# Kernel tuning notes

Hardware: AMD Instinct MI355X
Metric: run time of the kernel (lower is better)

Reference implementation:

```python
import jax, jax.numpy as jnp
import numpy as np

B, T, IN, H = 16, 256, 512, 1024
G = 4 * H  # gates: i, f, g, o (PyTorch order)
N_LAYERS = 8  # lstm1 (4 layers) + lstm2 (4 layers), all hidden=1024


def lstm_layer(x, Wih, Whh, bih, bhh):
    # x: [B,T,D_in]; Wih: [4H,D_in]; Whh: [4H,H]; biases: [4H]
    xg = jnp.einsum('btd,gd->btg', x, Wih) + bih + bhh  # precompute input proj [B,T,4H]
    b = x.shape[0]

    def step(carry, xg_t):
        h, c = carry
        g = xg_t + h @ Whh.T  # [B,4H]
        i, f, gg, o = jnp.split(g, 4, axis=-1)
        c = jax.nn.sigmoid(f) * c + jax.nn.sigmoid(i) * jnp.tanh(gg)
        h = jax.nn.sigmoid(o) * jnp.tanh(c)
        return (h, c), h

    init = (jnp.zeros((b, H), x.dtype), jnp.zeros((b, H), x.dtype))
    _, hs = jax.lax.scan(step, init, jnp.swapaxes(xg, 0, 1))  # [T,B,H]
    return jnp.swapaxes(hs, 0, 1)


def setup_inputs() -> dict:
    key = jax.random.key(0)
    ks = jax.random.split(key, 16)
    s = 1.0 / np.sqrt(H)  # PyTorch LSTM uniform init scale
    u = lambda k, shp: jax.random.uniform(k, shp, jnp.float32, -s, s)
    return {
        'x': jax.random.normal(ks[0], (B, T, IN), jnp.float32),
        'W_ih0': u(ks[1], (G, IN)),            # layer 0 input proj
        'W_ih_rest': u(ks[2], (N_LAYERS - 1, G, H)),  # layers 1..7
        'W_hh': u(ks[3], (N_LAYERS, G, H)),
        'b_ih': u(ks[4], (N_LAYERS, G)),
        'b_hh': u(ks[5], (N_LAYERS, G)),
        'fc1_w': u(ks[6], (512, H)), 'fc1_b': u(ks[7], (512,)),
        'fc2_w': u(ks[8], (256, 512)), 'fc2_b': u(ks[9], (256,)),
        'fc3_w': u(ks[10], (1, 256)), 'fc3_b': u(ks[11], (1,)),
    }


def reference(x, W_ih0, W_ih_rest, W_hh, b_ih, b_hh,
              fc1_w, fc1_b, fc2_w, fc2_b, fc3_w, fc3_b):
    # 8 stacked LSTM layers (dropout = identity in eval mode)
    h = lstm_layer(x, W_ih0, W_hh[0], b_ih[0], b_hh[0])
    for l in range(1, N_LAYERS):
        h = lstm_layer(h, W_ih_rest[l - 1], W_hh[l], b_ih[l], b_hh[l])
    out = h[:, -1, :]  # last timestep [B,H]
    out = jax.nn.relu(out @ fc1_w.T + fc1_b)
    out = jax.nn.relu(out @ fc2_w.T + fc2_b)
    return out @ fc3_w.T + fc3_b  # [B,1]
```

## Files before the change

### kernel.cpp

```cpp
#include <hip/hip_runtime.h>

constexpr int BB = 16;
constexpr int TT = 256;
constexpr int IN0 = 512;
constexpr int HH = 1024;
constexpr int GG = 4096;
constexpr int NLAYERS = 8;

constexpr size_t XG_OFF   = 0;
constexpr size_t REG0_OFF = 67108864;
constexpr size_t REG1_OFF = REG0_OFF + 16777216;
constexpr size_t HE_OFF   = REG1_OFF + 16777216;
constexpr size_t HO_OFF   = HE_OFF + 262144;
constexpr size_t FC1_OFF  = HO_OFF + 262144;
constexpr size_t FC2_OFF  = FC1_OFF + 32768;
constexpr size_t BAR_OFF  = FC2_OFF + 16384;

constexpr int BLO_B  = 69632;
constexpr int PART_F = 34816;
constexpr int SMEM_BYTES = 147968;

typedef __attribute__((ext_vector_type(8))) short bf16x8;
typedef __attribute__((ext_vector_type(4))) float f32x4;

__device__ __forceinline__ unsigned short f2bf(float f)
{
    union { float f; unsigned u; } v{f};
    unsigned r = v.u + 0x7FFFu + ((v.u >> 16) & 1u);
    return (unsigned short)(r >> 16);
}
__device__ __forceinline__ float bf2f(unsigned short h)
{
    union { unsigned u; float f; } v{(unsigned)h << 16};
    return v.f;
}

__global__ __launch_bounds__(256) void conv_split(const float* __restrict__ in,
                                                  ushort* __restrict__ oh,
                                                  ushort* __restrict__ ol, int n4)
{
    int g = blockIdx.x * blockDim.x + threadIdx.x;
    if (g >= n4) return;
    float4 f = ((const float4*)in)[g];
    ushort4 h, l;
    h.x = f2bf(f.x); l.x = f2bf(f.x - bf2f(h.x));
    h.y = f2bf(f.y); l.y = f2bf(f.y - bf2f(h.y));
    h.z = f2bf(f.z); l.z = f2bf(f.z - bf2f(h.z));
    h.w = f2bf(f.w); l.w = f2bf(f.w - bf2f(h.w));
    ((ushort4*)oh)[g] = h;
    ((ushort4*)ol)[g] = l;
}

__global__ __launch_bounds__(256) void gemm_mfma(const ushort* __restrict__ Ah,
                                                 const ushort* __restrict__ Al,
                                                 const ushort* __restrict__ Wh,
                                                 const ushort* __restrict__ Wl,
                                                 const float* __restrict__ bih,
                                                 const float* __restrict__ bhh,
                                                 float* __restrict__ out, int K)
{
    __shared__ ushort lds[2][128 * 72];
    const int tid = threadIdx.x;
    const int w = tid >> 6, ln = tid & 63;
    const int m0 = blockIdx.y * 128, n0 = blockIdx.x * 128;
    const int arow = (w >> 1) * 64, bcol = (w & 1) * 64;
    const int lm = ln & 15, lk = (ln >> 4) * 8;
    const int sr = tid >> 3, sc = (tid & 7) * 8;

    f32x4 acc[4][4] = {};

#pragma unroll
    for (int s = 0; s < 3; ++s) {
        const ushort* Asrc = (s < 2) ? Ah : Al;
        const ushort* Bsrc = (s == 1) ? Wl : Wh;
        for (int k0 = 0; k0 < K; k0 += 64) {
            __syncthreads();
#pragma unroll
            for (int i = 0; i < 4; ++i) {
                int r = sr + 32 * i;
                *(uint4*)&lds[0][r * 72 + sc] =
                    *(const uint4*)(Asrc + (size_t)(m0 + r) * K + k0 + sc);
                *(uint4*)&lds[1][r * 72 + sc] =
                    *(const uint4*)(Bsrc + (size_t)(n0 + r) * K + k0 + sc);
            }
            __syncthreads();
#pragma unroll
            for (int ks = 0; ks < 2; ++ks) {
                bf16x8 af[4], bf[4];
#pragma unroll
                for (int i = 0; i < 4; ++i)
                    af[i] = *(const bf16x8*)&lds[0][(arow + i * 16 + lm) * 72 + ks * 32 + lk];
#pragma unroll
                for (int j = 0; j < 4; ++j)
                    bf[j] = *(const bf16x8*)&lds[1][(bcol + j * 16 + lm) * 72 + ks * 32 + lk];
#pragma unroll
                for (int i = 0; i < 4; ++i)
#pragma unroll
                    for (int j = 0; j < 4; ++j)
                        acc[i][j] = __builtin_amdgcn_mfma_f32_16x16x32_bf16(
                            af[i], bf[j], acc[i][j], 0, 0, 0);
            }
        }
    }

#pragma unroll
    for (int j = 0; j < 4; ++j) {
        const int n = n0 + bcol + j * 16 + lm;
        const float bsum = bih[n] + bhh[n];
#pragma unroll
        for (int i = 0; i < 4; ++i) {
            const int mrow = m0 + arow + i * 16 + (ln >> 4) * 4;
#pragma unroll
            for (int r = 0; r < 4; ++r) {
                const int m = mrow + r;
                const int bb = m >> 8, tt = m & 255;
                out[(size_t)(tt * 16 + bb) * GG + n] = acc[i][j][r] + bsum;
            }
        }
    }
}

__device__ __forceinline__ float sigf(float x) { return 1.0f / (1.0f + expf(-x)); }

__global__ __launch_bounds__(512, 1) void scan_pair(
    const float* __restrict__ WhhE, const float* __restrict__ WhhO,
    const float* __restrict__ WihO, const float* __restrict__ xg,
    ushort* __restrict__ hseq_hi, ushort* __restrict__ hseq_lo,
    unsigned* __restrict__ hEbuf, unsigned* __restrict__ hObuf,
    const float* __restrict__ bihO, const float* __restrict__ bhhO,
    unsigned* __restrict__ barE, unsigned* __restrict__ barO,
    unsigned base)
{
    extern __shared__ float smem[];
    char* smb = (char*)smem;
    const int tid  = threadIdx.x;
    const int wgid = blockIdx.x;
    const int half = wgid >> 7, lwg = wgid & 127;
    const int j0 = lwg << 3;
    const int w = tid >> 6, ln = tid & 63;
    const int m = ln & 15, kq = ln >> 4;
    const int t_w = w & 1, s_w = w >> 1;
    const int grp = lwg >> 4;

    unsigned* myBar = half ? barO : barE;
    unsigned* otBar = half ? barE : barO;
    unsigned* myH   = half ? hObuf : hEbuf;

    bf16x8 wf_hi[8], wf_lo[8];
    {
        const int r = t_w * 16 + m;
        const int grow = ((r >> 3) << 10) + j0 + (r & 7);
        const float* wrow = (half ? WhhO : WhhE) + (size_t)grow * 1024 + (s_w << 8) + (kq << 3);
#pragma unroll
        for (int s = 0; s < 8; ++s) {
            float4 f0 = *(const float4*)(wrow + s * 32);
            float4 f1 = *(const float4*)(wrow + s * 32 + 4);
            float fv[8] = {f0.x, f0.y, f0.z, f0.w, f1.x, f1.y, f1.z, f1.w};
            bf16x8 h8, l8;
#pragma unroll
            for (int i = 0; i < 8; ++i) {
                unsigned short hb = f2bf(fv[i]);
                h8[i] = (short)hb;
                l8[i] = (short)f2bf(fv[i] - bf2f(hb));
            }
            wf_hi[s] = h8; wf_lo[s] = l8;
        }
    }
    bf16x8 uf_hi[8], uf_lo[8];
    if (half) {
        const int r = t_w * 16 + m;
        const int grow = ((r >> 3) << 10) + j0 + (r & 7);
        const float* wrow = WihO + (size_t)grow * 1024 + (s_w << 8) + (kq << 3);
#pragma unroll
        for (int s = 0; s < 8; ++s) {
            float4 f0 = *(const float4*)(wrow + s * 32);
            float4 f1 = *(const float4*)(wrow + s * 32 + 4);
            float fv[8] = {f0.x, f0.y, f0.z, f0.w, f1.x, f1.y, f1.z, f1.w};
            bf16x8 h8, l8;
#pragma unroll
            for (int i = 0; i < 8; ++i) {
                unsigned short hb = f2bf(fv[i]);
                h8[i] = (short)hb;
                l8[i] = (short)f2bf(fv[i] - bf2f(hb));
            }
            uf_hi[s] = h8; uf_lo[s] = l8;
        }
    }

    const int bidx = ln >> 4, jj = ln & 15;
    const int kkloc = jj >> 1, sub = (jj & 1) * 8;
    const int q = tid >> 4, bg = tid & 15;

    float cs0 = 0.f, cs1 = 0.f;
    float2 gin[4] = {};
    if (tid < 64) {
        if (half) {
#pragma unroll
            for (int g = 0; g < 4; ++g) {
                const int c0 = g * 1024 + j0 + 2 * q;
                gin[g] = make_float2(bihO[c0] + bhhO[c0], bihO[c0 + 1] + bhhO[c0 + 1]);
            }
        } else {
#pragma unroll
            for (int g = 0; g < 4; ++g)
                gin[g] = *(const float2*)(xg + (size_t)bg * GG + g * 1024 + j0 + 2 * q);
        }
    }

    for (int t = 0; t < TT; ++t) {
        const unsigned gt = base + (unsigned)t;
        if (tid == 0) {
            if (t > 0) {
                unsigned* p = myBar + 512 + (grp << 4);
                while (__hip_atomic_load(p, __ATOMIC_RELAXED, __HIP_MEMORY_SCOPE_AGENT) < gt)
                    __builtin_amdgcn_s_sleep(1);
            }
            if (half) {
                unsigned* p = otBar + 512 + (grp << 4);
                while (__hip_atomic_load(p, __ATOMIC_RELAXED, __HIP_MEMORY_SCOPE_AGENT) < gt + 1u)
                    __builtin_amdgcn_s_sleep(1);
            } else if (t >= 4) {
                unsigned* p = otBar + 512 + (grp << 4);
                while (__hip_atomic_load(p, __ATOMIC_RELAXED, __HIP_MEMORY_SCOPE_AGENT) < gt - 3u)
                    __builtin_amdgcn_s_sleep(1);
            }
        }
        __syncthreads();

        uint4 vE[2][4], vR[2][4];
        if (half) {
            const uint4* pEb = (const uint4*)(hEbuf + ((unsigned)(t & 3) << 14));
#pragma unroll
            for (int cc = 0; cc < 2; ++cc) {
                const uint4* p = pEb + ((w << 1) + cc) * 256 + ln;
                asm volatile(
                    "global_load_dwordx4 %0, %4, off sc0 sc1\n\t"
                    "global_load_dwordx4 %1, %4, off offset:1024 sc0 sc1\n\t"
                    "global_load_dwordx4 %2, %4, off offset:2048 sc0 sc1\n\t"
                    "global_load_dwordx4 %3, %4, off offset:3072 sc0 sc1"
                    : "=&v"(vE[cc][0]), "=&v"(vE[cc][1]), "=&v"(vE[cc][2]), "=&v"(vE[cc][3])
                    : "v"(p) : "memory");
            }
        }
        if (t > 0) {
            const uint4* pRb = (const uint4*)(myH + ((unsigned)((t - 1) & 3) << 14));
#pragma unroll
            for (int cc = 0; cc < 2; ++cc) {
                const uint4* p = pRb + ((w << 1) + cc) * 256 + ln;
                asm volatile(
                    "global_load_dwordx4 %0, %4, off sc0 sc1\n\t"
                    "global_load_dwordx4 %1, %4, off offset:1024 sc0 sc1\n\t"
                    "global_load_dwordx4 %2, %4, off offset:2048 sc0 sc1\n\t"
                    "global_load_dwordx4 %3, %4, off offset:3072 sc0 sc1"
                    : "=&v"(vR[cc][0]), "=&v"(vR[cc][1]), "=&v"(vR[cc][2]), "=&v"(vR[cc][3])
                    : "v"(p) : "memory");
            }
        }
        if (half || t > 0) {
            asm volatile("s_waitcnt vmcnt(0)" ::: "memory");
            __builtin_amdgcn_sched_barrier(0);
        }
        if (half) {
#pragma unroll
            for (int cc = 0; cc < 2; ++cc) {
                const int kk = ((w << 1) + cc) * 8 + kkloc;
#pragma unroll
                for (int i = 0; i < 4; ++i) {
                    const int b = (i << 2) + bidx;
                    uint4 pv = vE[cc][i];
                    uint2 uh = {(pv.x & 0xFFFFu) | (pv.y << 16),
                                (pv.z & 0xFFFFu) | (pv.w << 16)};
                    uint2 ul = {(pv.x >> 16) | (pv.y & 0xFFFF0000u),
                                (pv.z >> 16) | (pv.w & 0xFFFF0000u)};
                    char* bp = smb + kk * 272 + b * 16 + sub;
                    *(uint2*)bp = uh;
                    *(uint2*)(bp + BLO_B) = ul;
                }
            }
        }
        if (t > 0) {
#pragma unroll
            for (int cc = 0; cc < 2; ++cc) {
                const int kk = 128 + ((w << 1) + cc) * 8 + kkloc;
#pragma unroll
                for (int i = 0; i < 4; ++i) {
                    const int b = (i << 2) + bidx;
                    uint4 pv = vR[cc][i];
                    uint2 uh = {(pv.x & 0xFFFFu) | (pv.y << 16),
                                (pv.z & 0xFFFFu) | (pv.w << 16)};
                    uint2 ul = {(pv.x >> 16) | (pv.y & 0xFFFF0000u),
                                (pv.z >> 16) | (pv.w & 0xFFFF0000u)};
                    char* bp = smb + kk * 272 + b * 16 + sub;
                    *(uint2*)bp = uh;
                    *(uint2*)(bp + BLO_B) = ul;
                }
            }
        }
        __syncthreads();

        f32x4 aA = {0.f, 0.f, 0.f, 0.f};
        f32x4 aB = {0.f, 0.f, 0.f, 0.f};
        f32x4 aC = {0.f, 0.f, 0.f, 0.f};
        const char* hbx = smb + ((s_w << 5) + kq) * 272 + m * 16;
        const char* hbr = hbx + 128 * 272;
        if (half) {
#pragma unroll
            for (int s = 0; s < 8; ++s) {
                bf16x8 bh = *(const bf16x8*)(hbx + s * 1088);
                bf16x8 bl = *(const bf16x8*)(hbx + BLO_B + s * 1088);
                aA = __builtin_amdgcn_mfma_f32_16x16x32_bf16(uf_hi[s], bh, aA, 0, 0, 0);
                aB = __builtin_amdgcn_mfma_f32_16x16x32_bf16(uf_hi[s], bl, aB, 0, 0, 0);
                aC = __builtin_amdgcn_mfma_f32_16x16x32_bf16(uf_lo[s], bh, aC, 0, 0, 0);
            }
        }
        if (t > 0) {
#pragma unroll
            for (int s = 0; s < 8; ++s) {
                bf16x8 bh = *(const bf16x8*)(hbr + s * 1088);
                bf16x8 bl = *(const bf16x8*)(hbr + BLO_B + s * 1088);
                aA = __builtin_amdgcn_mfma_f32_16x16x32_bf16(wf_hi[s], bh, aA, 0, 0, 0);
                aB = __builtin_amdgcn_mfma_f32_16x16x32_bf16(wf_hi[s], bl, aB, 0, 0, 0);
                aC = __builtin_amdgcn_mfma_f32_16x16x32_bf16(wf_lo[s], bh, aC, 0, 0, 0);
            }
        }
        f32x4 asum = aA + aB;
        asum = asum + aC;

#pragma unroll
        for (int r = 0; r < 4; ++r)
            smem[PART_F + w * 272 + ((kq << 2) + r) * 17 + m] = asum[r];
        __syncthreads();

        unsigned pk0 = 0, pk1 = 0;
        if (tid < 64) {
#pragma unroll
            for (int cc = 0; cc < 2; ++cc) {
                const int ch = 2 * q + cc;
                float iv = cc ? gin[0].y : gin[0].x;
                float fv = cc ? gin[1].y : gin[1].x;
                float gv = cc ? gin[2].y : gin[2].x;
                float ov = cc ? gin[3].y : gin[3].x;
#pragma unroll
                for (int s = 0; s < 4; ++s) {
                    iv += smem[PART_F + (2 * s    ) * 272 + (ch    ) * 17 + bg];
                    fv += smem[PART_F + (2 * s    ) * 272 + (ch + 8) * 17 + bg];
                    gv += smem[PART_F + (2 * s + 1) * 272 + (ch    ) * 17 + bg];
                    ov += smem[PART_F + (2 * s + 1) * 272 + (ch + 8) * 17 + bg];
                }
                float& cs = cc ? cs1 : cs0;
                cs = sigf(fv) * cs + sigf(iv) * tanhf(gv);
                float hval = sigf(ov) * tanhf(cs);
                unsigned short hh_ = f2bf(hval);
                unsigned short hl_ = f2bf(hval - bf2f(hh_));
                unsigned pk = (unsigned)hh_ | ((unsigned)hl_ << 16);
                if (cc) pk1 = pk; else pk0 = pk;
                const int col = j0 + ch;
                unsigned* hdst = myH + ((unsigned)(t & 3) << 14) +
                                 ((col >> 6) << 10) + (bg << 6) + (col & 63);
                asm volatile("global_store_dword %0, %1, off sc0 sc1"
                             :: "v"(hdst), "v"(pk) : "memory");
            }
        }

        if (tid == 0) {
            asm volatile("s_waitcnt vmcnt(0)" ::: "memory");
            const unsigned T = gt + 1u;
            unsigned a = __hip_atomic_fetch_add(myBar + (grp << 4), 1u,
                                                __ATOMIC_RELAXED, __HIP_MEMORY_SCOPE_AGENT);
            if (a == 16u * T - 1u) {
                unsigned ra = __hip_atomic_fetch_add(myBar + 256, 1u,
                                                     __ATOMIC_RELAXED, __HIP_MEMORY_SCOPE_AGENT);
                if (ra == 8u * T - 1u) {
#pragma unroll
                    for (int i = 0; i < 8; ++i)
                        __hip_atomic_store(myBar + 512 + (i << 4), T,
                                           __ATOMIC_RELAXED, __HIP_MEMORY_SCOPE_AGENT);
                }
            }
        }

        if (tid < 64) {
            if (half) {
#pragma unroll
                for (int cc = 0; cc < 2; ++cc) {
                    const int col = j0 + 2 * q + cc;
                    const unsigned pk = cc ? pk1 : pk0;
                    size_t idx = (size_t)(bg * TT + t) * HH + col;
                    hseq_hi[idx] = (ushort)(pk & 0xFFFFu);
                    hseq_lo[idx] = (ushort)(pk >> 16);
                }
            } else if (t + 1 < TT) {
#pragma unroll
                for (int g = 0; g < 4; ++g)
                    gin[g] = *(const float2*)(xg + (size_t)((t + 1) * 16 + bg) * GG +
                                              g * 1024 + j0 + 2 * q);
            }
        }
    }
}

__global__ void fc_relu_split(const ushort* __restrict__ ih, const ushort* __restrict__ il,
                              const float* __restrict__ w, const float* __restrict__ b,
                              float* __restrict__ out, int N, int K)
{
    int g = blockIdx.x * blockDim.x + threadIdx.x;
    if (g >= BB * N) return;
    int bi = g / N, n = g - bi * N;
    const ushort* ph = ih + (size_t)(bi * 256 + 255) * 1024;
    const ushort* pl = il + (size_t)(bi * 256 + 255) * 1024;
    const float* wp = w + (size_t)n * K;
    float s = 0.f;
    for (int k = 0; k < K; k += 4) {
        ushort4 uh = *(const ushort4*)(ph + k);
        ushort4 ul = *(const ushort4*)(pl + k);
        float4 qv = *(const float4*)(wp + k);
        s += (bf2f(uh.x) + bf2f(ul.x)) * qv.x + (bf2f(uh.y) + bf2f(ul.y)) * qv.y +
             (bf2f(uh.z) + bf2f(ul.z)) * qv.z + (bf2f(uh.w) + bf2f(ul.w)) * qv.w;
    }
    s += b[n];
    out[g] = fmaxf(s, 0.f);
}

__global__ void fc_relu(const float* __restrict__ in, const float* __restrict__ w,
                        const float* __restrict__ b, float* __restrict__ out,
                        int N, int K, int do_relu)
{
    int g = blockIdx.x * blockDim.x + threadIdx.x;
    if (g >= BB * N) return;
    int bi = g / N, n = g - bi * N;
    const float* ip = in + (size_t)bi * K;
    const float* wp = w + (size_t)n * K;
    float s = 0.f;
    for (int k = 0; k < K; k += 4) {
        float4 a = *(const float4*)(ip + k);
        float4 qv = *(const float4*)(wp + k);
        s += a.x * qv.x + a.y * qv.y + a.z * qv.z + a.w * qv.w;
    }
    s += b[n];
    if (do_relu) s = fmaxf(s, 0.f);
    out[g] = s;
}

extern "C" void kernel_launch(void* const* d_in, const int* in_sizes, int n_in,
                              void* d_out, int out_size, void* d_ws, size_t ws_size,
                              hipStream_t stream)
{
    const float* x    = (const float*)d_in[0];
    const float* Wih0 = (const float*)d_in[1];
    const float* WihR = (const float*)d_in[2];
    const float* Whh  = (const float*)d_in[3];
    const float* bih  = (const float*)d_in[4];
    const float* bhh  = (const float*)d_in[5];
    const float* fc1w = (const float*)d_in[6];
    const float* fc1b = (const float*)d_in[7];
    const float* fc2w = (const float*)d_in[8];
    const float* fc2b = (const float*)d_in[9];
    const float* fc3w = (const float*)d_in[10];
    const float* fc3b = (const float*)d_in[11];
    float* out = (float*)d_out;
    char* ws = (char*)d_ws;

    float* xg      = (float*)(ws + XG_OFF);
    ushort* reg0   = (ushort*)(ws + REG0_OFF);
    ushort* hs_hi  = (ushort*)(ws + REG1_OFF);
    ushort* hs_lo  = hs_hi + 4194304;
    unsigned* hE   = (unsigned*)(ws + HE_OFF);
    unsigned* hO   = (unsigned*)(ws + HO_OFF);
    float* fc1o    = (float*)(ws + FC1_OFF);
    float* fc2o    = (float*)(ws + FC2_OFF);
    unsigned* barE = (unsigned*)(ws + BAR_OFF);
    unsigned* barO = (unsigned*)(ws + BAR_OFF + 4096);

    (void)hipFuncSetAttribute((const void*)scan_pair,
                              hipFuncAttributeMaxDynamicSharedMemorySize, SMEM_BYTES);
    (void)hipMemsetAsync(ws + BAR_OFF, 0, 8192, stream);

    ushort* xcv_hi = reg0;
    ushort* xcv_lo = reg0 + 2097152;
    ushort* w0h    = reg0 + 4194304;
    ushort* w0l    = reg0 + 6291456;
    conv_split<<<2048, 256, 0, stream>>>(x, xcv_hi, xcv_lo, (BB * TT * IN0) / 4);
    conv_split<<<2048, 256, 0, stream>>>(Wih0, w0h, w0l, (GG * IN0) / 4);
    gemm_mfma<<<dim3(32, 32), 256, 0, stream>>>(xcv_hi, xcv_lo, w0h, w0l,
                                                bih, bhh, xg, IN0);

    for (int p = 0; p < 4; ++p) {
        if (p > 0) {
            const float* Wl = WihR + (size_t)(2 * p - 1) * GG * HH;
            conv_split<<<4096, 256, 0, stream>>>(Wl, reg0, reg0 + 4194304, (GG * HH) / 4);
            gemm_mfma<<<dim3(32, 32), 256, 0, stream>>>(
                hs_hi, hs_lo, reg0, reg0 + 4194304,
                bih + (size_t)(2 * p) * GG, bhh + (size_t)(2 * p) * GG, xg, HH);
        }
        const float* whhE = Whh + (size_t)(2 * p) * GG * HH;
        const float* whhO = Whh + (size_t)(2 * p + 1) * GG * HH;
        const float* wihO = WihR + (size_t)(2 * p) * GG * HH;
        const float* bO   = bih + (size_t)(2 * p + 1) * GG;
        const float* bhO  = bhh + (size_t)(2 * p + 1) * GG;
        unsigned base = 256u * (unsigned)p;
        void* args[13] = {(void*)&whhE, (void*)&whhO, (void*)&wihO, (void*)&xg,
                          (void*)&hs_hi, (void*)&hs_lo, (void*)&hE, (void*)&hO,
                          (void*)&bO, (void*)&bhO, (void*)&barE, (void*)&barO,
                          (void*)&base};
        hipError_t e = hipLaunchCooperativeKernel((void*)scan_pair, dim3(256), dim3(512),
                                                  args, SMEM_BYTES, stream);
        if (e != hipSuccess) {
            scan_pair<<<dim3(256), dim3(512), SMEM_BYTES, stream>>>(
                whhE, whhO, wihO, xg, hs_hi, hs_lo, hE, hO, bO, bhO, barE, barO, base);
        }
    }

    fc_relu_split<<<32, 256, 0, stream>>>(hs_hi, hs_lo, fc1w, fc1b, fc1o, 512, 1024);
    fc_relu<<<16, 256, 0, stream>>>(fc1o, fc2w, fc2b, fc2o, 256, 512, 1);
    fc_relu<<<1, 16, 0, stream>>>(fc2o, fc3w, fc3b, out, 1, 256, 0);
}
```

Baseline: 7.387 ms.

## Replace hierarchical atomic barriers with parity-tagged hidden-state polling

The per-step global barrier built from grouped atomic counters is removed. Each packed hidden value now carries an epoch parity bit in the lowest bit of its low bf16 part, and consumers spin-reload the hidden-state ring buffer until every element shows the expected parity. A lightweight per-workgroup progress counter guards ring-buffer reuse between the two pipelined layers. This takes the atomic round trips and barrier latency off the serial recurrence critical path, at the cost of extra polling traffic and one bit of precision in the low-order hidden correction term.

```diff
diff --git a/kernel.cpp b/kernel.cpp
--- a/kernel.cpp
+++ b/kernel.cpp
@@ -14,7 +14,7 @@
 constexpr size_t HO_OFF   = HE_OFF + 262144;
 constexpr size_t FC1_OFF  = HO_OFF + 262144;
 constexpr size_t FC2_OFF  = FC1_OFF + 32768;
-constexpr size_t BAR_OFF  = FC2_OFF + 16384;
+constexpr size_t PRG_OFF  = FC2_OFF + 16384;
 
 constexpr int BLO_B  = 69632;
 constexpr int PART_F = 34816;
@@ -128,8 +128,7 @@
     ushort* __restrict__ hseq_hi, ushort* __restrict__ hseq_lo,
     unsigned* __restrict__ hEbuf, unsigned* __restrict__ hObuf,
     const float* __restrict__ bihO, const float* __restrict__ bhhO,
-    unsigned* __restrict__ barE, unsigned* __restrict__ barO,
-    unsigned base)
+    unsigned* __restrict__ prog, unsigned base)
 {
     extern __shared__ float smem[];
     char* smb = (char*)smem;
@@ -140,11 +139,8 @@
     const int w = tid >> 6, ln = tid & 63;
     const int m = ln & 15, kq = ln >> 4;
     const int t_w = w & 1, s_w = w >> 1;
-    const int grp = lwg >> 4;
-
-    unsigned* myBar = half ? barO : barE;
-    unsigned* otBar = half ? barE : barO;
-    unsigned* myH   = half ? hObuf : hEbuf;
+
+    unsigned* myH = half ? hObuf : hEbuf;
 
     bf16x8 wf_hi[8], wf_lo[8];
     {
@@ -208,58 +204,69 @@
     }
 
     for (int t = 0; t < TT; ++t) {
-        const unsigned gt = base + (unsigned)t;
-        if (tid == 0) {
-            if (t > 0) {
-                unsigned* p = myBar + 512 + (grp << 4);
-                while (__hip_atomic_load(p, __ATOMIC_RELAXED, __HIP_MEMORY_SCOPE_AGENT) < gt)
-                    __builtin_amdgcn_s_sleep(1);
-            }
-            if (half) {
-                unsigned* p = otBar + 512 + (grp << 4);
-                while (__hip_atomic_load(p, __ATOMIC_RELAXED, __HIP_MEMORY_SCOPE_AGENT) < gt + 1u)
-                    __builtin_amdgcn_s_sleep(1);
-            } else if (t >= 4) {
-                unsigned* p = otBar + 512 + (grp << 4);
-                while (__hip_atomic_load(p, __ATOMIC_RELAXED, __HIP_MEMORY_SCOPE_AGENT) < gt - 3u)
-                    __builtin_amdgcn_s_sleep(1);
-            }
-        }
-        __syncthreads();
+        const unsigned gstep = base + (unsigned)t;
+        const unsigned eE = (gstep >> 2) & 1u;
+        const unsigned eR = ((gstep - 1u) >> 2) & 1u;
 
         uint4 vE[2][4], vR[2][4];
-        if (half) {
-            const uint4* pEb = (const uint4*)(hEbuf + ((unsigned)(t & 3) << 14));
-#pragma unroll
-            for (int cc = 0; cc < 2; ++cc) {
-                const uint4* p = pEb + ((w << 1) + cc) * 256 + ln;
-                asm volatile(
-                    "global_load_dwordx4 %0, %4, off sc0 sc1\n\t"
-                    "global_load_dwordx4 %1, %4, off offset:1024 sc0 sc1\n\t"
-                    "global_load_dwordx4 %2, %4, off offset:2048 sc0 sc1\n\t"
-                    "global_load_dwordx4 %3, %4, off offset:3072 sc0 sc1"
-                    : "=&v"(vE[cc][0]), "=&v"(vE[cc][1]), "=&v"(vE[cc][2]), "=&v"(vE[cc][3])
-                    : "v"(p) : "memory");
-            }
-        }
-        if (t > 0) {
-            const uint4* pRb = (const uint4*)(myH + ((unsigned)((t - 1) & 3) << 14));
-#pragma unroll
-            for (int cc = 0; cc < 2; ++cc) {
-                const uint4* p = pRb + ((w << 1) + cc) * 256 + ln;
-                asm volatile(
-                    "global_load_dwordx4 %0, %4, off sc0 sc1\n\t"
-                    "global_load_dwordx4 %1, %4, off offset:1024 sc0 sc1\n\t"
-                    "global_load_dwordx4 %2, %4, off offset:2048 sc0 sc1\n\t"
-                    "global_load_dwordx4 %3, %4, off offset:3072 sc0 sc1"
-                    : "=&v"(vR[cc][0]), "=&v"(vR[cc][1]), "=&v"(vR[cc][2]), "=&v"(vR[cc][3])
-                    : "v"(p) : "memory");
-            }
-        }
         if (half || t > 0) {
-            asm volatile("s_waitcnt vmcnt(0)" ::: "memory");
-            __builtin_amdgcn_sched_barrier(0);
-        }
+            const uint4* pEb = (const uint4*)(hEbuf + ((gstep & 3u) << 14));
+            const uint4* pRb = (const uint4*)(myH + (((gstep - 1u) & 3u) << 14));
+            while (true) {
+                if (half) {
+#pragma unroll
+                    for (int cc = 0; cc < 2; ++cc) {
+                        const uint4* p = pEb + ((w << 1) + cc) * 256 + ln;
+                        asm volatile(
+                            "global_load_dwordx4 %0, %4, off sc0 sc1\n\t"
+                            "global_load_dwordx4 %1, %4, off offset:1024 sc0 sc1\n\t"
+                            "global_load_dwordx4 %2, %4, off offset:2048 sc0 sc1\n\t"
+                            "global_load_dwordx4 %3, %4, off offset:3072 sc0 sc1"
+                            : "=&v"(vE[cc][0]), "=&v"(vE[cc][1]), "=&v"(vE[cc][2]), "=&v"(vE[cc][3])
+                            : "v"(p) : "memory");
+                    }
+                }
+                if (t > 0) {
+#pragma unroll
+                    for (int cc = 0; cc < 2; ++cc) {
+                        const uint4* p = pRb + ((w << 1) + cc) * 256 + ln;
+                        asm volatile(
+                            "global_load_dwordx4 %0, %4, off sc0 sc1\n\t"
+                            "global_load_dwordx4 %1, %4, off offset:1024 sc0 sc1\n\t"
+                            "global_load_dwordx4 %2, %4, off offset:2048 sc0 sc1\n\t"
+                            "global_load_dwordx4 %3, %4, off offset:3072 sc0 sc1"
+                            : "=&v"(vR[cc][0]), "=&v"(vR[cc][1]), "=&v"(vR[cc][2]), "=&v"(vR[cc][3])
+                            : "v"(p) : "memory");
+                    }
+                }
+                asm volatile("s_waitcnt vmcnt(0)" ::: "memory");
+                __builtin_amdgcn_sched_barrier(0);
+                unsigned bad = 0u;
+                if (half) {
+#pragma unroll
+                    for (int cc = 0; cc < 2; ++cc)
+#pragma unroll
+                        for (int i = 0; i < 4; ++i) {
+                            uint4 v = vE[cc][i];
+                            bad |= ((v.x >> 16) ^ eE) & 1u; bad |= ((v.y >> 16) ^ eE) & 1u;
+                            bad |= ((v.z >> 16) ^ eE) & 1u; bad |= ((v.w >> 16) ^ eE) & 1u;
+                        }
+                }
+                if (t > 0) {
+#pragma unroll
+                    for (int cc = 0; cc < 2; ++cc)
+#pragma unroll
+                        for (int i = 0; i < 4; ++i) {
+                            uint4 v = vR[cc][i];
+                            bad |= ((v.x >> 16) ^ eR) & 1u; bad |= ((v.y >> 16) ^ eR) & 1u;
+                            bad |= ((v.z >> 16) ^ eR) & 1u; bad |= ((v.w >> 16) ^ eR) & 1u;
+                        }
+                }
+                if (__all(bad == 0u)) break;
+                __builtin_amdgcn_s_sleep(1);
+            }
+        }
+
         if (half) {
 #pragma unroll
             for (int cc = 0; cc < 2; ++cc) {
@@ -298,6 +305,10 @@
         }
         __syncthreads();
 
+        if (half && tid == 0)
+            __hip_atomic_store(prog + (lwg << 4), gstep + 1u,
+                               __ATOMIC_RELAXED, __HIP_MEMORY_SCOPE_AGENT);
+
         f32x4 aA = {0.f, 0.f, 0.f, 0.f};
         f32x4 aB = {0.f, 0.f, 0.f, 0.f};
         f32x4 aC = {0.f, 0.f, 0.f, 0.f};
@@ -331,7 +342,12 @@
             smem[PART_F + w * 272 + ((kq << 2) + r) * 17 + m] = asum[r];
         __syncthreads();
 
-        unsigned pk0 = 0, pk1 = 0;
+        if (!half && t >= 4 && tid == 0) {
+            unsigned* p = prog + (lwg << 4);
+            while (__hip_atomic_load(p, __ATOMIC_RELAXED, __HIP_MEMORY_SCOPE_AGENT) < gstep - 3u)
+                __builtin_amdgcn_s_sleep(1);
+        }
+
         if (tid < 64) {
 #pragma unroll
             for (int cc = 0; cc < 2; ++cc) {
@@ -352,44 +368,21 @@
                 float hval = sigf(ov) * tanhf(cs);
                 unsigned short hh_ = f2bf(hval);
                 unsigned short hl_ = f2bf(hval - bf2f(hh_));
-                unsigned pk = (unsigned)hh_ | ((unsigned)hl_ << 16);
-                if (cc) pk1 = pk; else pk0 = pk;
+                if (half) {
+                    const int col = j0 + ch;
+                    size_t idx = (size_t)(bg * TT + t) * HH + col;
+                    hseq_hi[idx] = hh_;
+                    hseq_lo[idx] = hl_;
+                }
+                unsigned short hlt = (unsigned short)((hl_ & 0xFFFEu) | ((gstep >> 2) & 1u));
+                unsigned pk = (unsigned)hh_ | ((unsigned)hlt << 16);
                 const int col = j0 + ch;
-                unsigned* hdst = myH + ((unsigned)(t & 3) << 14) +
+                unsigned* hdst = myH + ((gstep & 3u) << 14) +
                                  ((col >> 6) << 10) + (bg << 6) + (col & 63);
                 asm volatile("global_store_dword %0, %1, off sc0 sc1"
                              :: "v"(hdst), "v"(pk) : "memory");
             }
-        }
-
-        if (tid == 0) {
-            asm volatile("s_waitcnt vmcnt(0)" ::: "memory");
-            const unsigned T = gt + 1u;
-            unsigned a = __hip_atomic_fetch_add(myBar + (grp << 4), 1u,
-                                                __ATOMIC_RELAXED, __HIP_MEMORY_SCOPE_AGENT);
-            if (a == 16u * T - 1u) {
-                unsigned ra = __hip_atomic_fetch_add(myBar + 256, 1u,
-                                                     __ATOMIC_RELAXED, __HIP_MEMORY_SCOPE_AGENT);
-                if (ra == 8u * T - 1u) {
-#pragma unroll
-                    for (int i = 0; i < 8; ++i)
-                        __hip_atomic_store(myBar + 512 + (i << 4), T,
-                                           __ATOMIC_RELAXED, __HIP_MEMORY_SCOPE_AGENT);
-                }
-            }
-        }
-
-        if (tid < 64) {
-            if (half) {
-#pragma unroll
-                for (int cc = 0; cc < 2; ++cc) {
-                    const int col = j0 + 2 * q + cc;
-                    const unsigned pk = cc ? pk1 : pk0;
-                    size_t idx = (size_t)(bg * TT + t) * HH + col;
-                    hseq_hi[idx] = (ushort)(pk & 0xFFFFu);
-                    hseq_lo[idx] = (ushort)(pk >> 16);
-                }
-            } else if (t + 1 < TT) {
+            if (!half && t + 1 < TT) {
 #pragma unroll
                 for (int g = 0; g < 4; ++g)
                     gin[g] = *(const float2*)(xg + (size_t)((t + 1) * 16 + bg) * GG +
@@ -468,12 +461,12 @@
     unsigned* hO   = (unsigned*)(ws + HO_OFF);
     float* fc1o    = (float*)(ws + FC1_OFF);
     float* fc2o    = (float*)(ws + FC2_OFF);
-    unsigned* barE = (unsigned*)(ws + BAR_OFF);
-    unsigned* barO = (unsigned*)(ws + BAR_OFF + 4096);
+    unsigned* prog = (unsigned*)(ws + PRG_OFF);
 
     (void)hipFuncSetAttribute((const void*)scan_pair,
                               hipFuncAttributeMaxDynamicSharedMemorySize, SMEM_BYTES);
-    (void)hipMemsetAsync(ws + BAR_OFF, 0, 8192, stream);
+    (void)hipMemsetAsync(ws + HE_OFF, 0xFF, 524288, stream);
+    (void)hipMemsetAsync(ws + PRG_OFF, 0, 8192, stream);
 
     ushort* xcv_hi = reg0;
     ushort* xcv_lo = reg0 + 2097152;
@@ -498,15 +491,14 @@
         const float* bO   = bih + (size_t)(2 * p + 1) * GG;
         const float* bhO  = bhh + (size_t)(2 * p + 1) * GG;
         unsigned base = 256u * (unsigned)p;
-        void* args[13] = {(void*)&whhE, (void*)&whhO, (void*)&wihO, (void*)&xg,
+        void* args[12] = {(void*)&whhE, (void*)&whhO, (void*)&wihO, (void*)&xg,
                           (void*)&hs_hi, (void*)&hs_lo, (void*)&hE, (void*)&hO,
-                          (void*)&bO, (void*)&bhO, (void*)&barE, (void*)&barO,
-                          (void*)&base};
+                          (void*)&bO, (void*)&bhO, (void*)&prog, (void*)&base};
         hipError_t e = hipLaunchCooperativeKernel((void*)scan_pair, dim3(256), dim3(512),
                                                   args, SMEM_BYTES, stream);
         if (e != hipSuccess) {
             scan_pair<<<dim3(256), dim3(512), SMEM_BYTES, stream>>>(
-                whhE, whhO, wihO, xg, hs_hi, hs_lo, hE, hO, bO, bhO, barE, barO, base);
+                whhE, whhO, wihO, xg, hs_hi, hs_lo, hE, hO, bO, bhO, prog, base);
         }
     }
 
```

After: 13.40 ms. +81.4%, slower.
